# Performance work log

Measured on AMD Instinct MI355X. Metric: run time of the kernel, lower is better.

## Reference

```python
import jax, jax.numpy as jnp
import numpy as np
from jax import lax

B, C, OUT, K, L = 8, 256, 256, 7, 2048
STRIDE, PAD, DIL = 1, 3, 1

def setup_inputs() -> dict:
    key = jax.random.key(0)
    k1, k2, k3, k4, k5 = jax.random.split(key, 5)
    return {
        "x": jax.random.normal(k1, (B, C, L), jnp.float32),
        "w_off": jax.random.normal(k2, (C * K * 2, C, K), jnp.float32) * 0.02,
        "b_off": jax.random.normal(k3, (C * K * 2,), jnp.float32) * 0.02,
        "weight": jax.random.normal(k4, (OUT, C, K), jnp.float32) * 0.02,
        "bias": jax.random.normal(k5, (OUT,), jnp.float32) * 0.02,
    }

def _gather_lin(x, idx):
    # x: (B,C,Lin), idx: (B,C,K,Lout) -> zero-padded gather along length
    Lin = x.shape[-1]
    valid = (idx >= 0) & (idx < Lin)
    idxc = jnp.clip(idx, 0, Lin - 1)
    v = jnp.take_along_axis(x[:, :, None, :], idxc, axis=3)
    return jnp.where(valid, v, jnp.zeros((), x.dtype))

def reference(x, w_off, b_off, weight, bias):
    # offset/mask predictor conv (same geometry as main conv)
    off = lax.conv_general_dilated(
        x, w_off, window_strides=(STRIDE,), padding=[(PAD, PAD)],
        rhs_dilation=(DIL,), dimension_numbers=("NCH", "OIH", "NCH"))
    off = off + b_off[None, :, None]
    Lout = off.shape[-1]
    off = off.reshape(B, 2, C * K, Lout)
    offset = off[:, 0].reshape(B, C, K, Lout)          # fractional shift per (c,k,p)
    mask = jax.nn.sigmoid(off[:, 1]).reshape(B, C, K, Lout)
    # base sampling grid: p*stride - pad + k*dil
    base = (jnp.arange(Lout) * STRIDE - PAD)[None, :] + (jnp.arange(K) * DIL)[:, None]  # (K,Lout)
    pos = offset + base[None, None].astype(x.dtype)    # (B,C,K,Lout)
    p0 = jnp.floor(pos)
    frac = pos - p0
    p0i = p0.astype(jnp.int32)
    sampled = _gather_lin(x, p0i) * (1.0 - frac) + _gather_lin(x, p0i + 1) * frac
    sampled = sampled * mask
    # grouped conv accumulate (groups=1): (B,C,K,L) x (O,C,K) -> (B,O,L)
    out = jnp.einsum("bckl,ock->bol", sampled, weight) + bias[None, :, None]
    return out
```

## Files before the change

### kernel.cpp

```cpp
#include <hip/hip_runtime.h>

typedef unsigned short ushort_t;
typedef __attribute__((ext_vector_type(8))) short bf16x8;
typedef __attribute__((ext_vector_type(4))) float f32x4;
typedef __attribute__((ext_vector_type(8))) unsigned short ushort8;

constexpr int BB   = 8;
constexpr int CC   = 256;
constexpr int OUTC = 256;
constexpr int KK   = 7;
constexpr int LL   = 2048;
constexpr int PADc = 3;
constexpr int KD   = CC * KK;
constexpr int MOFF = CC * KK * 2;
constexpr int NTOT = BB * LL;
constexpr int NKSTEPS = KD / 32;
constexpr int LP   = LL + 6;
constexpr int BUFU = 12288;

__device__ __forceinline__ ushort_t f2bf(float f) {
    unsigned u = __float_as_uint(f);
    unsigned r = (u + 0x7fffu + ((u >> 16) & 1u)) >> 16;
    return (ushort_t)r;
}

__global__ __launch_bounds__(256) void cast_k(const float4* __restrict__ src,
                                              ushort_t* __restrict__ dst, int n4) {
    int i = blockIdx.x * 256 + threadIdx.x;
    if (i >= n4) return;
    float4 v = src[i];
    ushort4 o;
    o.x = f2bf(v.x); o.y = f2bf(v.y); o.z = f2bf(v.z); o.w = f2bf(v.w);
    *(ushort4*)(dst + (size_t)i * 4) = o;
}

__global__ __launch_bounds__(256) void castperm_woff(const float* __restrict__ src,
                                                     ushort_t* __restrict__ dst) {
    int i = blockIdx.x * 256 + threadIdx.x;
    if (i >= MOFF * KD) return;
    int dr  = i / KD;
    int q   = i - dr * KD;
    int cs   = q / 224;
    int r224 = q - cs * 224;
    int tap  = r224 >> 5;
    int cl   = r224 & 31;
    int c = cs * 32 + cl;
    int r = (dr & 1) ? (KD + (dr >> 1)) : (dr >> 1);
    dst[i] = f2bf(src[(r * 256 + c) * 7 + tap]);
}

__global__ __launch_bounds__(256) void xpose_k(const float* __restrict__ x,
                                               ushort_t* __restrict__ xp) {
    __shared__ float tile[32][257];
    int bid = blockIdx.x;
    int b  = bid >> 6;
    int l0 = ((bid >> 3) & 7) * 256;
    int c0 = (bid & 7) * 32;
    int tid = threadIdx.x;
    const float* xb = x + (size_t)b * (CC * LL);
    ushort_t* xpb = xp + (size_t)b * (LP * 256);
#pragma unroll 4
    for (int k = 0; k < 32; ++k)
        tile[k][tid] = xb[(size_t)(c0 + k) * LL + l0 + tid];
    __syncthreads();
    int lp = l0 + tid + 3;
#pragma unroll
    for (int q = 0; q < 8; ++q) {
        ushort4 v;
        v.x = f2bf(tile[4 * q + 0][tid]);
        v.y = f2bf(tile[4 * q + 1][tid]);
        v.z = f2bf(tile[4 * q + 2][tid]);
        v.w = f2bf(tile[4 * q + 3][tid]);
        *(ushort4*)(xpb + (size_t)lp * 256 + c0 + 4 * q) = v;
    }
    if ((bid & 63) == 0) {
#pragma unroll
        for (int r = 0; r < 6; ++r) {
            int glp = (r < 3) ? r : (2048 + r);
            xpb[glp * 256 + tid] = 0;
        }
    }
}

__device__ __forceinline__ void load_lds16(const ushort_t* g, ushort_t* l) {
    __builtin_amdgcn_global_load_lds(
        (const __attribute__((address_space(1))) unsigned int*)g,
        (__attribute__((address_space(3))) unsigned int*)l, 16, 0, 0);
}

__device__ __forceinline__ void stageA128(ushort_t* ldsbuf,
                                          const ushort_t* __restrict__ A,
                                          int m0, int kt, int tid) {
    int g = (tid & 3) ^ ((tid >> 3) & 3);
    int row = tid >> 2;
    load_lds16(A + (size_t)(m0 + row) * KD + kt * 32 + g * 8,
               ldsbuf + (tid >> 6) * 512);
}
__device__ __forceinline__ void stageB256(ushort_t* ldsbuf,
                                          const ushort_t* __restrict__ xp,
                                          int n0, int kt, int tid) {
    int g = (tid & 3) ^ ((tid >> 3) & 3);
    int cs = kt / 7;
    int tap = kt - cs * 7;
    const ushort_t* base = xp + (size_t)(n0 >> 11) * (LP * 256)
                              + (size_t)((n0 & 2047) + tap) * 256 + cs * 32 + g * 8;
#pragma unroll
    for (int j = 0; j < 2; ++j) {
        int row = j * 128 + (tid >> 2);
        load_lds16(base + (size_t)row * 256,
                   ldsbuf + 4096 + j * 4096 + (tid >> 6) * 512);
    }
}

template <int VMC, bool PF>
__device__ __forceinline__ void kstepN(const ushort_t* __restrict__ A,
                                       const ushort_t* __restrict__ xp,
                                       ushort_t* lds, int m0, int n0, int kt,
                                       int tid, int wr, int wc,
                                       int r15, int u, f32x4 (&acc)[4][4]) {
    asm volatile("s_waitcnt vmcnt(%0)" :: "n"(VMC) : "memory");
    __builtin_amdgcn_s_barrier();
    const ushort_t* buf = lds + (size_t)(kt % 3) * BUFU;
    const ushort_t* pa = buf + (wr * 64 + r15) * 32 + u * 8;
    const ushort_t* pb = buf + 4096 + (wc * 64 + r15) * 32 + u * 8;
    bf16x8 af[4], bq[4];
#pragma unroll
    for (int i = 0; i < 4; ++i) af[i] = *(const bf16x8*)(pa + i * 512);
#pragma unroll
    for (int j = 0; j < 4; ++j) bq[j] = *(const bf16x8*)(pb + j * 512);
    if (PF) {
        ushort_t* nb = lds + (size_t)((kt + 2) % 3) * BUFU;
        stageA128(nb, A,  m0, kt + 2, tid);
        stageB256(nb, xp, n0, kt + 2, tid);
    }
    __builtin_amdgcn_s_setprio(1);
#pragma unroll
    for (int i = 0; i < 4; ++i)
#pragma unroll
        for (int j = 0; j < 4; ++j)
            acc[i][j] = __builtin_amdgcn_mfma_f32_16x16x32_bf16(af[i], bq[j], acc[i][j], 0, 0, 0);
    __builtin_amdgcn_s_setprio(0);
}

__global__ __launch_bounds__(512, 4) void gemm128n_off_fused(const ushort_t* __restrict__ A,
                                                             const ushort_t* __restrict__ xp,
                                                             const float* __restrict__ boff,
                                                             const float* __restrict__ x,
                                                             ushort_t* __restrict__ s) {
    __shared__ __align__(16) ushort_t lds[3 * BUFU];
    constexpr int NT = NTOT / 256;
    constexpr int NWG = (MOFF / 128) * NT;
    int bid = blockIdx.x;
    int wg = (bid & 7) * (NWG / 8) + (bid >> 3);
    int mt = wg / NT, nt = wg % NT;
    int m0 = mt * 128, n0 = nt * 256;
    int tid = threadIdx.x, wid = tid >> 6, lane = tid & 63;
    int wr = wid >> 2, wc = wid & 3;
    int r15 = lane & 15, kh = lane >> 4;
    int u = kh ^ ((r15 >> 1) & 3);

    f32x4 acc[4][4] = {};

    stageA128(lds,        A,  m0, 0, tid);
    stageB256(lds,        xp, n0, 0, tid);
    stageA128(lds + BUFU, A,  m0, 1, tid);
    stageB256(lds + BUFU, xp, n0, 1, tid);

    for (int kt = 0; kt < NKSTEPS - 2; ++kt)
        kstepN<3, true>(A, xp, lds, m0, n0, kt, tid, wr, wc, r15, u, acc);
    kstepN<3, false>(A, xp, lds, m0, n0, NKSTEPS - 2, tid, wr, wc, r15, u, acc);
    kstepN<0, false>(A, xp, lds, m0, n0, NKSTEPS - 1, tid, wr, wc, r15, u, acc);

    __syncthreads();
    ushort_t* st = lds;
#pragma unroll
    for (int i = 0; i < 4; ++i) {
        int mloc = wr * 64 + i * 16 + kh * 4;
        int ckb  = (m0 + mloc) >> 1;
        int ckl  = mloc >> 1;
        float bo0 = boff[ckb],     bm0 = boff[KD + ckb];
        float bo1 = boff[ckb + 1], bm1 = boff[KD + ckb + 1];
        int c0 = ckb / 7,       kk0 = ckb - c0 * 7;
        int c1 = (ckb + 1) / 7, kk1 = (ckb + 1) - c1 * 7;
#pragma unroll
        for (int j = 0; j < 4; ++j) {
            int nl = wc * 64 + j * 16 + r15;
            int n = n0 + nl;
            int b = n >> 11, l = n & 2047;
            const float* xb_ = x + (size_t)b * (CC * LL);
            f32x4 v = acc[i][j];
            ushort2 o2;
#pragma unroll
            for (int p = 0; p < 2; ++p) {
                float offv = v[2 * p]     + (p ? bo1 : bo0);
                float mpre = v[2 * p + 1] + (p ? bm1 : bm0);
                int c = p ? c1 : c0, kk = p ? kk1 : kk0;
                float mask = 1.0f / (1.0f + __expf(-mpre));
                float pos = offv + (float)(l - PADc + kk);
                float p0f = floorf(pos);
                float frac = pos - p0f;
                int p0 = (int)p0f;
                const float* xr = xb_ + (size_t)c * LL;
                float x0 = ((unsigned)p0 < (unsigned)LL) ? xr[p0] : 0.0f;
                float x1 = ((unsigned)(p0 + 1) < (unsigned)LL) ? xr[p0 + 1] : 0.0f;
                float sv = (x0 + (x1 - x0) * frac) * mask;
                if (p) o2.y = f2bf(sv); else o2.x = f2bf(sv);
            }
            *(ushort2*)(st + nl * 72 + ckl) = o2;
        }
    }
    __syncthreads();
    int srow = tid >> 3;
    int scol = tid & 7;
    int ck0g = m0 >> 1;
#pragma unroll
    for (int pass = 0; pass < 4; ++pass) {
        int nl = pass * 64 + srow;
        ushort8 v8 = *(const ushort8*)(st + nl * 72 + scol * 8);
        *(ushort8*)(s + (size_t)(n0 + nl) * KD + ck0g + scol * 8) = v8;
    }
}

__device__ __forceinline__ void stage128(ushort_t* ldsbuf,
                                         const ushort_t* __restrict__ A,
                                         const ushort_t* __restrict__ Bt,
                                         int m0, int n0, int kt,
                                         int wid, int lane) {
    int t = wid * 64 + lane;
    int g = (t & 3) ^ ((t >> 3) & 3);
#pragma unroll
    for (int j = 0; j < 2; ++j) {
        int row = j * 64 + (t >> 2);
        load_lds16(A  + (size_t)(m0 + row) * KD + kt * 32 + g * 8,
                   ldsbuf + j * 2048 + wid * 512);
        load_lds16(Bt + (size_t)(n0 + row) * KD + kt * 32 + g * 8,
                   ldsbuf + 4096 + j * 2048 + wid * 512);
    }
}

template <int VMC>
__device__ __forceinline__ void kstep128(const ushort_t* __restrict__ A,
                                         const ushort_t* __restrict__ Bt,
                                         ushort_t* lds, int m0, int n0, int kt,
                                         int wid, int lane, int wr, int wc,
                                         int r15, int u, f32x4 (&acc)[4][4]) {
    asm volatile("s_waitcnt vmcnt(%0)" :: "n"(VMC) : "memory");
    __builtin_amdgcn_s_barrier();
    const ushort_t* buf = lds + (size_t)(kt & 3) * 8192;
    const ushort_t* pa = buf + (wr * 64 + r15) * 32 + u * 8;
    const ushort_t* pb = buf + 4096 + (wc * 64 + r15) * 32 + u * 8;
    bf16x8 af[4], bq[4];
#pragma unroll
    for (int i = 0; i < 4; ++i) af[i] = *(const bf16x8*)(pa + i * 512);
#pragma unroll
    for (int j = 0; j < 4; ++j) bq[j] = *(const bf16x8*)(pb + j * 512);
    if (kt + 3 < NKSTEPS)
        stage128(lds + (size_t)((kt + 3) & 3) * 8192, A, Bt, m0, n0, kt + 3, wid, lane);
    __builtin_amdgcn_s_setprio(1);
#pragma unroll
    for (int i = 0; i < 4; ++i)
#pragma unroll
        for (int j = 0; j < 4; ++j)
            acc[i][j] = __builtin_amdgcn_mfma_f32_16x16x32_bf16(af[i], bq[j], acc[i][j], 0, 0, 0);
    __builtin_amdgcn_s_setprio(0);
}

__global__ __launch_bounds__(256, 2) void gemm128_out(const ushort_t* __restrict__ A,
                                                      const ushort_t* __restrict__ Bt,
                                                      const float* __restrict__ bvec,
                                                      float* __restrict__ Dout) {
    __shared__ __align__(16) ushort_t lds[4 * 8192];
    constexpr int NT = NTOT / 128;
    constexpr int NWG = (OUTC / 128) * NT;
    int bid = blockIdx.x;
    int wg = (bid & 7) * (NWG / 8) + (bid >> 3);
    int mt = wg / NT, nt = wg % NT;
    int m0 = mt * 128, n0 = nt * 128;
    int tid = threadIdx.x, wid = tid >> 6, lane = tid & 63;
    int wr = wid >> 1, wc = wid & 1;
    int r15 = lane & 15, kh = lane >> 4;
    int u = kh ^ ((r15 >> 1) & 3);

    f32x4 acc[4][4] = {};

    stage128(lds,            A, Bt, m0, n0, 0, wid, lane);
    stage128(lds + 8192,     A, Bt, m0, n0, 1, wid, lane);
    stage128(lds + 2 * 8192, A, Bt, m0, n0, 2, wid, lane);

    for (int kt = 0; kt < NKSTEPS - 2; ++kt)
        kstep128<8>(A, Bt, lds, m0, n0, kt, wid, lane, wr, wc, r15, u, acc);
    kstep128<4>(A, Bt, lds, m0, n0, NKSTEPS - 2, wid, lane, wr, wc, r15, u, acc);
    kstep128<0>(A, Bt, lds, m0, n0, NKSTEPS - 1, wid, lane, wr, wc, r15, u, acc);

    int rbase = kh * 4;
#pragma unroll
    for (int i = 0; i < 4; ++i)
#pragma unroll
        for (int j = 0; j < 4; ++j) {
            int m = m0 + wr * 64 + i * 16 + rbase;
            int n = n0 + wc * 64 + j * 16 + r15;
            int b = n >> 11, l = n & 2047;
#pragma unroll
            for (int r = 0; r < 4; ++r) {
                float val = acc[i][j][r] + bvec[m + r];
                Dout[((size_t)(b * OUTC + (m + r))) * LL + l] = val;
            }
        }
}

extern "C" void kernel_launch(void* const* d_in, const int* in_sizes, int n_in,
                              void* d_out, int out_size, void* d_ws, size_t ws_size,
                              hipStream_t stream) {
    const float* x      = (const float*)d_in[0];
    const float* w_off  = (const float*)d_in[1];
    const float* b_off  = (const float*)d_in[2];
    const float* weight = (const float*)d_in[3];
    const float* bias   = (const float*)d_in[4];
    float* out = (float*)d_out;

    ushort_t* w = (ushort_t*)d_ws;
    ushort_t* wb  = w;
    ushort_t* wtb = wb  + MOFF * KD;
    ushort_t* xp  = wtb + OUTC * KD;
    ushort_t* s   = xp  + BB * LP * 256;

    castperm_woff<<<(MOFF * KD + 255) / 256, 256, 0, stream>>>(w_off, wb);
    cast_k<<<(114688 + 255) / 256, 256, 0, stream>>>((const float4*)weight, wtb, 114688);
    xpose_k<<<512, 256, 0, stream>>>(x, xp);

    gemm128n_off_fused<<<(MOFF / 128) * (NTOT / 256), 512, 0, stream>>>(wb, xp, b_off, x, s);

    gemm128_out<<<(OUTC / 128) * (NTOT / 128), 256, 0, stream>>>(wtb, s, bias, out);
}
```

Baseline: 265.9 us.

## Use 4-wave 128x256 tiles with register double-buffered fragments in offset GEMM

The fused offset GEMM now runs 256 threads per block instead of 512. Each wave computes a 128x64 sub-tile, so it holds 8x4 accumulators instead of 4x4. LDS fragments are read into two alternating register sets, so the reads for the next k-step are issued before the MFMAs of the current step, and global prefetch is placed between two barriers. The aim is more MFMA work per LDS read and overlap of LDS latency with compute. In exchange, register pressure roughly doubles, occupancy is lower, and each step has an extra barrier.

```diff
diff --git a/kernel.cpp b/kernel.cpp
--- a/kernel.cpp
+++ b/kernel.cpp
@@ -88,61 +88,72 @@
         (__attribute__((address_space(3))) unsigned int*)l, 16, 0, 0);
 }
 
-__device__ __forceinline__ void stageA128(ushort_t* ldsbuf,
-                                          const ushort_t* __restrict__ A,
-                                          int m0, int kt, int tid) {
+__device__ __forceinline__ void stageAp(ushort_t* ldsbuf, const ushort_t* __restrict__ A,
+                                        int m0, int kt, int tid) {
     int g = (tid & 3) ^ ((tid >> 3) & 3);
-    int row = tid >> 2;
-    load_lds16(A + (size_t)(m0 + row) * KD + kt * 32 + g * 8,
-               ldsbuf + (tid >> 6) * 512);
-}
-__device__ __forceinline__ void stageB256(ushort_t* ldsbuf,
-                                          const ushort_t* __restrict__ xp,
-                                          int n0, int kt, int tid) {
+    int w = tid >> 6;
+#pragma unroll
+    for (int j = 0; j < 2; ++j) {
+        int row = j * 64 + (tid >> 2);
+        load_lds16(A + (size_t)(m0 + row) * KD + kt * 32 + g * 8,
+                   ldsbuf + j * 2048 + w * 512);
+    }
+}
+__device__ __forceinline__ void stageBp(ushort_t* ldsbuf, const ushort_t* __restrict__ xp,
+                                        int n0, int kt, int tid) {
     int g = (tid & 3) ^ ((tid >> 3) & 3);
-    int cs = kt / 7;
-    int tap = kt - cs * 7;
+    int cs = kt / 7, tap = kt - cs * 7;
     const ushort_t* base = xp + (size_t)(n0 >> 11) * (LP * 256)
                               + (size_t)((n0 & 2047) + tap) * 256 + cs * 32 + g * 8;
-#pragma unroll
-    for (int j = 0; j < 2; ++j) {
-        int row = j * 128 + (tid >> 2);
-        load_lds16(base + (size_t)row * 256,
-                   ldsbuf + 4096 + j * 4096 + (tid >> 6) * 512);
-    }
-}
-
-template <int VMC, bool PF>
-__device__ __forceinline__ void kstepN(const ushort_t* __restrict__ A,
+    int w = tid >> 6;
+#pragma unroll
+    for (int j = 0; j < 4; ++j) {
+        int row = j * 64 + (tid >> 2);
+        load_lds16(base + (size_t)row * 256, ldsbuf + 4096 + j * 2048 + w * 512);
+    }
+}
+
+__device__ __forceinline__ void readFrags(const ushort_t* buf, int wc, int r15, int u,
+                                          bf16x8 (&af)[8], bf16x8 (&bq)[4]) {
+    const ushort_t* pa = buf + r15 * 32 + u * 8;
+    const ushort_t* pb = buf + 4096 + (wc * 64 + r15) * 32 + u * 8;
+#pragma unroll
+    for (int i = 0; i < 8; ++i) af[i] = *(const bf16x8*)(pa + i * 512);
+#pragma unroll
+    for (int j = 0; j < 4; ++j) bq[j] = *(const bf16x8*)(pb + j * 512);
+}
+
+template <int MODE>
+__device__ __forceinline__ void kstepP(const ushort_t* __restrict__ A,
                                        const ushort_t* __restrict__ xp,
                                        ushort_t* lds, int m0, int n0, int kt,
-                                       int tid, int wr, int wc,
-                                       int r15, int u, f32x4 (&acc)[4][4]) {
-    asm volatile("s_waitcnt vmcnt(%0)" :: "n"(VMC) : "memory");
-    __builtin_amdgcn_s_barrier();
-    const ushort_t* buf = lds + (size_t)(kt % 3) * BUFU;
-    const ushort_t* pa = buf + (wr * 64 + r15) * 32 + u * 8;
-    const ushort_t* pb = buf + 4096 + (wc * 64 + r15) * 32 + u * 8;
-    bf16x8 af[4], bq[4];
-#pragma unroll
-    for (int i = 0; i < 4; ++i) af[i] = *(const bf16x8*)(pa + i * 512);
-#pragma unroll
-    for (int j = 0; j < 4; ++j) bq[j] = *(const bf16x8*)(pb + j * 512);
-    if (PF) {
-        ushort_t* nb = lds + (size_t)((kt + 2) % 3) * BUFU;
-        stageA128(nb, A,  m0, kt + 2, tid);
-        stageB256(nb, xp, n0, kt + 2, tid);
+                                       int tid, int wc, int r15, int u,
+                                       bf16x8 (&afC)[8], bf16x8 (&bqC)[4],
+                                       bf16x8 (&afP)[8], bf16x8 (&bqP)[4],
+                                       f32x4 (&acc)[8][4]) {
+    if (MODE != 2) {
+        __builtin_amdgcn_s_barrier();
+        if (MODE == 0) {
+            ushort_t* nb = lds + (size_t)((kt + 2) % 3) * BUFU;
+            stageAp(nb, A,  m0, kt + 2, tid);
+            stageBp(nb, xp, n0, kt + 2, tid);
+            asm volatile("s_waitcnt vmcnt(6)" ::: "memory");
+        } else {
+            asm volatile("s_waitcnt vmcnt(0)" ::: "memory");
+        }
+        __builtin_amdgcn_s_barrier();
+        readFrags(lds + (size_t)((kt + 1) % 3) * BUFU, wc, r15, u, afP, bqP);
     }
     __builtin_amdgcn_s_setprio(1);
 #pragma unroll
-    for (int i = 0; i < 4; ++i)
+    for (int i = 0; i < 8; ++i)
 #pragma unroll
         for (int j = 0; j < 4; ++j)
-            acc[i][j] = __builtin_amdgcn_mfma_f32_16x16x32_bf16(af[i], bq[j], acc[i][j], 0, 0, 0);
+            acc[i][j] = __builtin_amdgcn_mfma_f32_16x16x32_bf16(afC[i], bqC[j], acc[i][j], 0, 0, 0);
     __builtin_amdgcn_s_setprio(0);
 }
 
-__global__ __launch_bounds__(512, 4) void gemm128n_off_fused(const ushort_t* __restrict__ A,
+__global__ __launch_bounds__(256, 2) void gemm128p_off_fused(const ushort_t* __restrict__ A,
                                                              const ushort_t* __restrict__ xp,
                                                              const float* __restrict__ boff,
                                                              const float* __restrict__ x,
@@ -154,28 +165,35 @@
     int wg = (bid & 7) * (NWG / 8) + (bid >> 3);
     int mt = wg / NT, nt = wg % NT;
     int m0 = mt * 128, n0 = nt * 256;
-    int tid = threadIdx.x, wid = tid >> 6, lane = tid & 63;
-    int wr = wid >> 2, wc = wid & 3;
+    int tid = threadIdx.x, lane = tid & 63;
+    int wc = tid >> 6;
     int r15 = lane & 15, kh = lane >> 4;
     int u = kh ^ ((r15 >> 1) & 3);
 
-    f32x4 acc[4][4] = {};
-
-    stageA128(lds,        A,  m0, 0, tid);
-    stageB256(lds,        xp, n0, 0, tid);
-    stageA128(lds + BUFU, A,  m0, 1, tid);
-    stageB256(lds + BUFU, xp, n0, 1, tid);
-
-    for (int kt = 0; kt < NKSTEPS - 2; ++kt)
-        kstepN<3, true>(A, xp, lds, m0, n0, kt, tid, wr, wc, r15, u, acc);
-    kstepN<3, false>(A, xp, lds, m0, n0, NKSTEPS - 2, tid, wr, wc, r15, u, acc);
-    kstepN<0, false>(A, xp, lds, m0, n0, NKSTEPS - 1, tid, wr, wc, r15, u, acc);
+    f32x4 acc[8][4] = {};
+    bf16x8 afA[8], bqA[4], afB[8], bqB[4];
+
+    stageAp(lds,        A,  m0, 0, tid);
+    stageBp(lds,        xp, n0, 0, tid);
+    stageAp(lds + BUFU, A,  m0, 1, tid);
+    stageBp(lds + BUFU, xp, n0, 1, tid);
+    asm volatile("s_waitcnt vmcnt(6)" ::: "memory");
+    __builtin_amdgcn_s_barrier();
+    readFrags(lds, wc, r15, u, afA, bqA);
+
+#pragma unroll 1
+    for (int p = 0; p < 27; ++p) {
+        kstepP<0>(A, xp, lds, m0, n0, 2 * p,     tid, wc, r15, u, afA, bqA, afB, bqB, acc);
+        kstepP<0>(A, xp, lds, m0, n0, 2 * p + 1, tid, wc, r15, u, afB, bqB, afA, bqA, acc);
+    }
+    kstepP<1>(A, xp, lds, m0, n0, 54, tid, wc, r15, u, afA, bqA, afB, bqB, acc);
+    kstepP<2>(A, xp, lds, m0, n0, 55, tid, wc, r15, u, afB, bqB, afA, bqA, acc);
 
     __syncthreads();
     ushort_t* st = lds;
 #pragma unroll
-    for (int i = 0; i < 4; ++i) {
-        int mloc = wr * 64 + i * 16 + kh * 4;
+    for (int i = 0; i < 8; ++i) {
+        int mloc = i * 16 + kh * 4;
         int ckb  = (m0 + mloc) >> 1;
         int ckl  = mloc >> 1;
         float bo0 = boff[ckb],     bm0 = boff[KD + ckb];
@@ -214,8 +232,8 @@
     int scol = tid & 7;
     int ck0g = m0 >> 1;
 #pragma unroll
-    for (int pass = 0; pass < 4; ++pass) {
-        int nl = pass * 64 + srow;
+    for (int pass = 0; pass < 8; ++pass) {
+        int nl = pass * 32 + srow;
         ushort8 v8 = *(const ushort8*)(st + nl * 72 + scol * 8);
         *(ushort8*)(s + (size_t)(n0 + nl) * KD + ck0g + scol * 8) = v8;
     }
@@ -238,13 +256,13 @@
     }
 }
 
-template <int VMC>
+template <int VMCN>
 __device__ __forceinline__ void kstep128(const ushort_t* __restrict__ A,
                                          const ushort_t* __restrict__ Bt,
                                          ushort_t* lds, int m0, int n0, int kt,
                                          int wid, int lane, int wr, int wc,
                                          int r15, int u, f32x4 (&acc)[4][4]) {
-    asm volatile("s_waitcnt vmcnt(%0)" :: "n"(VMC) : "memory");
+    asm volatile("s_waitcnt vmcnt(%0)" :: "n"(VMCN) : "memory");
     __builtin_amdgcn_s_barrier();
     const ushort_t* buf = lds + (size_t)(kt & 3) * 8192;
     const ushort_t* pa = buf + (wr * 64 + r15) * 32 + u * 8;
@@ -328,7 +346,7 @@
     cast_k<<<(114688 + 255) / 256, 256, 0, stream>>>((const float4*)weight, wtb, 114688);
     xpose_k<<<512, 256, 0, stream>>>(x, xp);
 
-    gemm128n_off_fused<<<(MOFF / 128) * (NTOT / 256), 512, 0, stream>>>(wb, xp, b_off, x, s);
+    gemm128p_off_fused<<<(MOFF / 128) * (NTOT / 256), 256, 0, stream>>>(wb, xp, b_off, x, s);
 
     gemm128_out<<<(OUTC / 128) * (NTOT / 128), 256, 0, stream>>>(wtb, s, bias, out);
 }
```

New measurement: 280.2 us. +5.4%, slower.

## Load B operand directly from global into registers in offset GEMM

Applied to the files above, without the earlier changes.

The offset-predictor GEMM no longer stages the B (transposed input) tile through LDS. Each wave loads its own B fragments straight from global memory into registers, double-buffered across k-steps, while only A is staged through a three-buffer LDS ring. This cuts LDS capacity and traffic and moves the barrier to after the MFMA block with explicit vmcnt waits. The cost is uncoalesced per-lane 16-byte global loads that rely on cache reuse, since neighbouring waves read overlapping shifted rows for the convolution taps.

```diff
diff --git a/kernel.cpp b/kernel.cpp
--- a/kernel.cpp
+++ b/kernel.cpp
@@ -16,7 +16,7 @@
 constexpr int NTOT = BB * LL;
 constexpr int NKSTEPS = KD / 32;
 constexpr int LP   = LL + 6;
-constexpr int BUFU = 12288;
+constexpr int ABUF = 4096;
 
 __device__ __forceinline__ ushort_t f2bf(float f) {
     unsigned u = __float_as_uint(f);
@@ -88,66 +88,57 @@
         (__attribute__((address_space(3))) unsigned int*)l, 16, 0, 0);
 }
 
-__device__ __forceinline__ void stageA128(ushort_t* ldsbuf,
-                                          const ushort_t* __restrict__ A,
-                                          int m0, int kt, int tid) {
+__device__ __forceinline__ void stageAp(ushort_t* ldsbuf, const ushort_t* __restrict__ A,
+                                        int m0, int kt, int tid) {
     int g = (tid & 3) ^ ((tid >> 3) & 3);
     int row = tid >> 2;
     load_lds16(A + (size_t)(m0 + row) * KD + kt * 32 + g * 8,
                ldsbuf + (tid >> 6) * 512);
 }
-__device__ __forceinline__ void stageB256(ushort_t* ldsbuf,
-                                          const ushort_t* __restrict__ xp,
-                                          int n0, int kt, int tid) {
-    int g = (tid & 3) ^ ((tid >> 3) & 3);
-    int cs = kt / 7;
-    int tap = kt - cs * 7;
-    const ushort_t* base = xp + (size_t)(n0 >> 11) * (LP * 256)
-                              + (size_t)((n0 & 2047) + tap) * 256 + cs * 32 + g * 8;
-#pragma unroll
-    for (int j = 0; j < 2; ++j) {
-        int row = j * 128 + (tid >> 2);
-        load_lds16(base + (size_t)row * 256,
-                   ldsbuf + 4096 + j * 4096 + (tid >> 6) * 512);
-    }
-}
-
-template <int VMC, bool PF>
-__device__ __forceinline__ void kstepN(const ushort_t* __restrict__ A,
-                                       const ushort_t* __restrict__ xp,
-                                       ushort_t* lds, int m0, int n0, int kt,
-                                       int tid, int wr, int wc,
-                                       int r15, int u, f32x4 (&acc)[4][4]) {
-    asm volatile("s_waitcnt vmcnt(%0)" :: "n"(VMC) : "memory");
-    __builtin_amdgcn_s_barrier();
-    const ushort_t* buf = lds + (size_t)(kt % 3) * BUFU;
-    const ushort_t* pa = buf + (wr * 64 + r15) * 32 + u * 8;
-    const ushort_t* pb = buf + 4096 + (wc * 64 + r15) * 32 + u * 8;
-    bf16x8 af[4], bq[4];
+
+__device__ __forceinline__ void loadB(bf16x8 (&bq)[4], const ushort_t* __restrict__ xpb,
+                                      int nrow, int kt, int kh) {
+    int cs = kt / 7, tap = kt - cs * 7;
+    const ushort_t* bb = xpb + (size_t)(nrow + tap) * 256 + cs * 32 + kh * 8;
+#pragma unroll
+    for (int j = 0; j < 4; ++j)
+        bq[j] = *(const bf16x8*)(bb + (size_t)j * 16 * 256);
+}
+
+template <int MODE>
+__device__ __forceinline__ void kstepR(const ushort_t* __restrict__ A,
+                                       const ushort_t* __restrict__ xpb,
+                                       ushort_t* lds, int m0, int nrow, int kt,
+                                       int tid, int wr, int r15, int kh, int u,
+                                       bf16x8 (&bqC)[4], bf16x8 (&bqN)[4],
+                                       f32x4 (&acc)[4][4]) {
+    const ushort_t* pa = lds + (size_t)(kt % 3) * ABUF + (wr * 64 + r15) * 32 + u * 8;
+    bf16x8 af[4];
 #pragma unroll
     for (int i = 0; i < 4; ++i) af[i] = *(const bf16x8*)(pa + i * 512);
-#pragma unroll
-    for (int j = 0; j < 4; ++j) bq[j] = *(const bf16x8*)(pb + j * 512);
-    if (PF) {
-        ushort_t* nb = lds + (size_t)((kt + 2) % 3) * BUFU;
-        stageA128(nb, A,  m0, kt + 2, tid);
-        stageB256(nb, xp, n0, kt + 2, tid);
-    }
+    if (MODE != 2) loadB(bqN, xpb, nrow, kt + 1, kh);
+    if (MODE == 0) stageAp(lds + (size_t)((kt + 2) % 3) * ABUF, A, m0, kt + 2, tid);
     __builtin_amdgcn_s_setprio(1);
 #pragma unroll
     for (int i = 0; i < 4; ++i)
 #pragma unroll
         for (int j = 0; j < 4; ++j)
-            acc[i][j] = __builtin_amdgcn_mfma_f32_16x16x32_bf16(af[i], bq[j], acc[i][j], 0, 0, 0);
+            acc[i][j] = __builtin_amdgcn_mfma_f32_16x16x32_bf16(af[i], bqC[j], acc[i][j], 0, 0, 0);
     __builtin_amdgcn_s_setprio(0);
-}
-
-__global__ __launch_bounds__(512, 4) void gemm128n_off_fused(const ushort_t* __restrict__ A,
+    if (MODE == 0)      asm volatile("s_waitcnt vmcnt(5)" ::: "memory");
+    else if (MODE == 1) asm volatile("s_waitcnt vmcnt(4)" ::: "memory");
+    if (MODE != 2) {
+        __builtin_amdgcn_sched_barrier(0);
+        __builtin_amdgcn_s_barrier();
+    }
+}
+
+__global__ __launch_bounds__(512, 4) void gemm128r_off_fused(const ushort_t* __restrict__ A,
                                                              const ushort_t* __restrict__ xp,
                                                              const float* __restrict__ boff,
                                                              const float* __restrict__ x,
                                                              ushort_t* __restrict__ s) {
-    __shared__ __align__(16) ushort_t lds[3 * BUFU];
+    __shared__ __align__(16) ushort_t lds[18432];
     constexpr int NT = NTOT / 256;
     constexpr int NWG = (MOFF / 128) * NT;
     int bid = blockIdx.x;
@@ -159,17 +150,26 @@
     int r15 = lane & 15, kh = lane >> 4;
     int u = kh ^ ((r15 >> 1) & 3);
 
+    const ushort_t* xpb = xp + (size_t)(n0 >> 11) * (LP * 256);
+    int nrow = (n0 & 2047) + wc * 64 + r15;
+
     f32x4 acc[4][4] = {};
-
-    stageA128(lds,        A,  m0, 0, tid);
-    stageB256(lds,        xp, n0, 0, tid);
-    stageA128(lds + BUFU, A,  m0, 1, tid);
-    stageB256(lds + BUFU, xp, n0, 1, tid);
-
-    for (int kt = 0; kt < NKSTEPS - 2; ++kt)
-        kstepN<3, true>(A, xp, lds, m0, n0, kt, tid, wr, wc, r15, u, acc);
-    kstepN<3, false>(A, xp, lds, m0, n0, NKSTEPS - 2, tid, wr, wc, r15, u, acc);
-    kstepN<0, false>(A, xp, lds, m0, n0, NKSTEPS - 1, tid, wr, wc, r15, u, acc);
+    bf16x8 bqA[4], bqB[4];
+
+    loadB(bqA, xpb, nrow, 0, kh);
+    stageAp(lds,        A, m0, 0, tid);
+    stageAp(lds + ABUF, A, m0, 1, tid);
+    asm volatile("s_waitcnt vmcnt(1)" ::: "memory");
+    __builtin_amdgcn_sched_barrier(0);
+    __builtin_amdgcn_s_barrier();
+
+#pragma unroll 1
+    for (int p = 0; p < 27; ++p) {
+        kstepR<0>(A, xpb, lds, m0, nrow, 2 * p,     tid, wr, r15, kh, u, bqA, bqB, acc);
+        kstepR<0>(A, xpb, lds, m0, nrow, 2 * p + 1, tid, wr, r15, kh, u, bqB, bqA, acc);
+    }
+    kstepR<1>(A, xpb, lds, m0, nrow, 54, tid, wr, r15, kh, u, bqA, bqB, acc);
+    kstepR<2>(A, xpb, lds, m0, nrow, 55, tid, wr, r15, kh, u, bqB, bqA, acc);
 
     __syncthreads();
     ushort_t* st = lds;
@@ -238,13 +238,13 @@
     }
 }
 
-template <int VMC>
+template <int VMCN>
 __device__ __forceinline__ void kstep128(const ushort_t* __restrict__ A,
                                          const ushort_t* __restrict__ Bt,
                                          ushort_t* lds, int m0, int n0, int kt,
                                          int wid, int lane, int wr, int wc,
                                          int r15, int u, f32x4 (&acc)[4][4]) {
-    asm volatile("s_waitcnt vmcnt(%0)" :: "n"(VMC) : "memory");
+    asm volatile("s_waitcnt vmcnt(%0)" :: "n"(VMCN) : "memory");
     __builtin_amdgcn_s_barrier();
     const ushort_t* buf = lds + (size_t)(kt & 3) * 8192;
     const ushort_t* pa = buf + (wr * 64 + r15) * 32 + u * 8;
@@ -328,7 +328,7 @@
     cast_k<<<(114688 + 255) / 256, 256, 0, stream>>>((const float4*)weight, wtb, 114688);
     xpose_k<<<512, 256, 0, stream>>>(x, xp);
 
-    gemm128n_off_fused<<<(MOFF / 128) * (NTOT / 256), 512, 0, stream>>>(wb, xp, b_off, x, s);
+    gemm128r_off_fused<<<(MOFF / 128) * (NTOT / 256), 512, 0, stream>>>(wb, xp, b_off, x, s);
 
     gemm128_out<<<(OUTC / 128) * (NTOT / 128), 256, 0, stream>>>(wtb, s, bias, out);
 }
```

New measurement: 462.3 us. 73.9% more time.
